# Optimization experiments

Hardware: AMD Instinct MI355X
Metric: run time of the kernel (lower is better)

The kernel has to match this reference:

```python
import jax, jax.numpy as jnp
import numpy as np

D = 512; N_HEAD = 8; D_HEAD = 64; D_INNER = 2048; SEG = 512; N_LAYER = 2; BATCH = 32
NUM_ITEMS = 50000
OMEGA = [2, 3, 4, 5, 7, 11, 21, 50]  # len == N_HEAD, required by multi-scale mask broadcast
EPS = 1e-8
STD = 0.02


def _layer_norm(x, w, b):
    mu = x.mean(-1, keepdims=True)
    var = ((x - mu) ** 2).mean(-1, keepdims=True)
    return (x - mu) / jnp.sqrt(var + EPS) * w + b


def _masks():
    # dir_mask: triu(ones, 1) (reverse=False); ms_mask[i,j,m] per omega band
    dir_mask = jnp.triu(jnp.ones((SEG, SEG), jnp.float32), 1)
    ms = np.stack([np.tri(SEG, SEG, o - 1) != np.tri(SEG, SEG, -o) for o in OMEGA], axis=-1)
    return dir_mask, jnp.asarray(ms)


def _pos_emb():
    freq = jnp.arange(0, D, 2, dtype=jnp.float32)
    inv_freq = 1.0 / jnp.power(10000.0, freq / D)
    pos_seq = jnp.arange(SEG, -SEG, -1.0, dtype=jnp.float32)  # length 2*SEG
    sinusoid = pos_seq[:, None] * inv_freq[None, :]
    return jnp.concatenate([jnp.sin(sinusoid), jnp.cos(sinusoid)], axis=-1)  # (2S, D)


def _rel_shift_bnij(x, klen):
    b, n, i, j2 = x.shape
    x = x.reshape(b, n, j2, i)[:, :, 1:, :].reshape(b, n, i, j2 - 1)
    return x[:, :, :, :klen]


def setup_inputs() -> dict:
    key = jax.random.key(0)
    ks = jax.random.split(key, 16)
    L = N_LAYER
    item_emb = STD * jax.random.normal(ks[0], (NUM_ITEMS + 1, D), jnp.float32)
    item_emb = item_emb.at[0].set(0.0)  # padding_idx=0
    proj = lambda k: STD * jax.random.normal(k, (L, D, N_HEAD, D_HEAD), jnp.float32)
    return {
        "input_ids": jax.random.randint(ks[1], (BATCH, SEG), 0, NUM_ITEMS + 1),
        "input_mask": jnp.zeros((BATCH, SEG), jnp.float32),
        "item_emb": item_emb,
        "Wq": proj(ks[2]), "Wk": proj(ks[3]), "Wv": proj(ks[4]),
        "Wr": proj(ks[5]), "Wo": proj(ks[6]),
        "r_r_bias": STD * jax.random.normal(ks[7], (L, N_HEAD, D_HEAD), jnp.float32),
        "r_w_bias": STD * jax.random.normal(ks[8], (L, N_HEAD, D_HEAD), jnp.float32),
        "ln_attn_w": jnp.ones((L, D), jnp.float32), "ln_attn_b": jnp.zeros((L, D), jnp.float32),
        "W1": STD * jax.random.normal(ks[9], (L, D, D_INNER), jnp.float32),
        "b1": jnp.zeros((L, D_INNER), jnp.float32),
        "W2": STD * jax.random.normal(ks[10], (L, D_INNER, D), jnp.float32),
        "b2": jnp.zeros((L, D), jnp.float32),
        "ln_ff_w": jnp.ones((L, D), jnp.float32), "ln_ff_b": jnp.zeros((L, D), jnp.float32),
    }


def reference(input_ids, input_mask, item_emb, Wq, Wk, Wv, Wr, Wo, r_r_bias, r_w_bias,
              ln_attn_w, ln_attn_b, W1, b1, W2, b2, ln_ff_w, ln_ff_b):
    ids = input_ids.T                      # (S, B)
    im = input_mask.T.astype(jnp.float32)  # (S, B)
    dir_mask, ms_mask = _masks()
    # data_mask: (q,k,b); attn_mask: (q,k,b,n) via multi-scale bands (training path)
    data_mask = im[None, :, :] + im[:, None, :] + dir_mask[:, :, None]
    attn_mask = ((data_mask[:, :, :, None] + (~ms_mask)[:, :, None, :].astype(jnp.float32)) > 0).astype(jnp.float32)
    mask_bnij = jnp.transpose(attn_mask, (2, 3, 0, 1))  # (b,n,i,j)

    h = item_emb[ids]          # (S, B, D)
    pos = _pos_emb()           # (2S, D), shared across batch
    scale = 1.0 / np.sqrt(D_HEAD).astype(np.float32)

    for l in range(N_LAYER):
        k_h = jnp.einsum('ibh,hnd->ibnd', h, Wk[l])
        v_h = jnp.einsum('ibh,hnd->ibnd', h, Wv[l])
        k_r = jnp.einsum('jh,hnd->jnd', pos, Wr[l])   # pos shared across batch
        q_h = jnp.einsum('ibh,hnd->ibnd', h, Wq[l])
        ac = jnp.einsum('ibnd,jbnd->bnij', q_h + r_w_bias[l], k_h)
        bd = jnp.einsum('ibnd,jnd->bnij', q_h + r_r_bias[l], k_r)
        bd = _rel_shift_bnij(bd, SEG)
        attn_score = (ac + bd) * scale - 1e30 * mask_bnij
        attn_prob = jax.nn.softmax(attn_score, axis=3)
        attn_vec = jnp.einsum('bnij,jbnd->ibnd', attn_prob, v_h)
        attn_out = jnp.einsum('ibnd,hnd->ibh', attn_vec, Wo[l])
        h = _layer_norm(attn_out + h, ln_attn_w[l], ln_attn_b[l])
        ff = jax.nn.gelu(h @ W1[l] + b1[l], approximate=False) @ W2[l] + b2[l]
        h = _layer_norm(ff + h, ln_ff_w[l], ln_ff_b[l])

    return jnp.transpose(h, (1, 0, 2))  # (B, S, D)
```

## Files before the change

kernel.cpp:

```cpp
#include <hip/hip_runtime.h>
#include <math.h>


#define S_  512
#define B_  32
#define D_  512
#define NH  8
#define DH  64
#define DI  2048
#define M_  (S_*B_)
#define QKV_LD 1536
#define WL  3407872
#define FP32_ONE 0x3F800000u

typedef unsigned short ushort_t;
typedef __attribute__((ext_vector_type(8))) short short8;
typedef __attribute__((ext_vector_type(4))) float f32x4;

__constant__ int OMEGA_C[8] = {2, 3, 4, 5, 7, 11, 21, 50};

__device__ __forceinline__ float b2f(ushort_t us) {
    return __uint_as_float(((unsigned int)us) << 16);
}
__device__ __forceinline__ ushort_t f2b(float f) {
    unsigned int u = __float_as_uint(f);
    return (ushort_t)((u + 0x7fffu + ((u >> 16) & 1u)) >> 16);
}
__device__ __forceinline__ float ldx(const void* p, size_t idx, bool isbf) {
    return isbf ? b2f(((const ushort_t*)p)[idx]) : ((const float*)p)[idx];
}
__device__ __forceinline__ void async16(const ushort_t* g, ushort_t* l) {
    __builtin_amdgcn_global_load_lds(
        (const __attribute__((address_space(1))) unsigned int*)g,
        (__attribute__((address_space(3))) unsigned int*)l, 16, 0, 0);
}

__device__ __forceinline__ float fast_gelu(float v) {
    float x  = v * 0.7071067811865475f;
    float ax = fabsf(x);
    float t  = __builtin_amdgcn_rcpf(fmaf(0.3275911f, ax, 1.f));
    float p  = fmaf(fmaf(fmaf(fmaf(1.061405429f, t, -1.453152027f),
                              t, 1.421413741f),
                         t, -0.284496736f),
                    t, 0.254829592f) * t;
    float e    = __expf(-ax * ax);
    float erfa = fmaf(-p, e, 1.f);
    float erfx = copysignf(erfa, x);
    return 0.5f * v * (1.f + erfx);
}

#define DPPA(v, ctrl) v += __int_as_float(__builtin_amdgcn_update_dpp(0, __float_as_int(v), ctrl, 0xf, 0xf, true))
__device__ __forceinline__ void dpp_sum64(float& v) {
    DPPA(v, 0x111); DPPA(v, 0x112); DPPA(v, 0x114);
    DPPA(v, 0x118); DPPA(v, 0x142); DPPA(v, 0x143);
}
#define DPPROR(v, ctrl) __int_as_float(__builtin_amdgcn_update_dpp(__float_as_int(v), __float_as_int(v), ctrl, 0xf, 0xf, false))
__device__ __forceinline__ float row16_sum(float v) {
    v += DPPROR(v, 0x128); v += DPPROR(v, 0x124);
    v += DPPROR(v, 0x122); v += DPPROR(v, 0x121);
    return v;
}
__device__ __forceinline__ float row16_max(float v) {
    v = fmaxf(v, DPPROR(v, 0x128)); v = fmaxf(v, DPPROR(v, 0x124));
    v = fmaxf(v, DPPROR(v, 0x122)); v = fmaxf(v, DPPROR(v, 0x121));
    return v;
}
__device__ __forceinline__ float rlane(float v, int l) {
    return __int_as_float(__builtin_amdgcn_readlane(__float_as_int(v), l));
}

__global__ __launch_bounds__(256) void embed_kernel(const int* __restrict__ ids,
                                                    const void* __restrict__ emb,
                                                    ushort_t* __restrict__ h,
                                                    const unsigned int* __restrict__ dtp) {
    const bool isbf = (dtp[0] != FP32_ONE);
    int idx = blockIdx.x * 256 + threadIdx.x;
    int d8 = idx & 63;
    int row = idx >> 6;
    int s = row >> 5, b = row & 31;
    int id = ids[b * S_ + s];
    size_t src = (size_t)id * D_ + d8 * 8;
    if (isbf) {
        *(uint4*)(h + (size_t)row * D_ + d8 * 8) = *(const uint4*)((const ushort_t*)emb + src);
    } else {
        const float* e = (const float*)emb + src;
        float4 a0 = ((const float4*)e)[0], a1 = ((const float4*)e)[1];
        uint4 pk;
        pk.x = (unsigned)f2b(a0.x) | ((unsigned)f2b(a0.y) << 16);
        pk.y = (unsigned)f2b(a0.z) | ((unsigned)f2b(a0.w) << 16);
        pk.z = (unsigned)f2b(a1.x) | ((unsigned)f2b(a1.y) << 16);
        pk.w = (unsigned)f2b(a1.z) | ((unsigned)f2b(a1.w) << 16);
        *(uint4*)(h + (size_t)row * D_ + d8 * 8) = pk;
    }
}

__global__ __launch_bounds__(256) void posemb_kernel(ushort_t* __restrict__ pos) {
    int flat = blockIdx.x * 256 + threadIdx.x;
    int p = flat >> 8, k = flat & 255;
    float inv = expf((float)k * -0.035977892078031f);
    float val = (512.0f - (float)p) * inv;
    pos[p * D_ + k]       = f2b(sinf(val));
    pos[p * D_ + 256 + k] = f2b(cosf(val));
}

__global__ __launch_bounds__(256) void transp_cvt4(
    const void* __restrict__ s0, const void* __restrict__ s1,
    const void* __restrict__ s2, const void* __restrict__ s3,
    ushort_t* __restrict__ wbuf, const unsigned int* __restrict__ dtp) {
    const bool isbf = (dtp[0] != FP32_ONE);
    __shared__ float tt[32][33];
    int z = blockIdx.z, layer = z >> 2, t4 = z & 3;
    const void* srcs[4] = {s0, s1, s2, s3};
    const void* in = srcs[t4];
    size_t inoff = (size_t)layer * 262144;
    ushort_t* out = wbuf + (size_t)layer * WL + (size_t)t4 * 262144;
    int tx = threadIdx.x & 31, ty = threadIdx.x >> 5;
    int n0 = blockIdx.x * 32, k0 = blockIdx.y * 32;
#pragma unroll
    for (int it = 0; it < 4; ++it)
        tt[ty + it * 8][tx] = ldx(in, inoff + (size_t)(k0 + ty + it * 8) * 512 + n0 + tx, isbf);
    __syncthreads();
#pragma unroll
    for (int it = 0; it < 4; ++it)
        out[(size_t)(n0 + ty + it * 8) * 512 + k0 + tx] = f2b(tt[tx][ty + it * 8]);
}

__global__ __launch_bounds__(256) void transp_cvtL(const void* __restrict__ in, size_t perlin,
                                                   ushort_t* __restrict__ wbuf, size_t outoff,
                                                   const unsigned int* __restrict__ dtp,
                                                   int K, int N) {
    const bool isbf = (dtp[0] != FP32_ONE);
    __shared__ float tt[32][33];
    int layer = blockIdx.z;
    size_t inoff = (size_t)layer * perlin;
    ushort_t* out = wbuf + (size_t)layer * WL + outoff;
    int tx = threadIdx.x & 31, ty = threadIdx.x >> 5;
    int n0 = blockIdx.x * 32, k0 = blockIdx.y * 32;
#pragma unroll
    for (int it = 0; it < 4; ++it)
        tt[ty + it * 8][tx] = ldx(in, inoff + (size_t)(k0 + ty + it * 8) * N + n0 + tx, isbf);
    __syncthreads();
#pragma unroll
    for (int it = 0; it < 4; ++it)
        out[(size_t)(n0 + ty + it * 8) * K + k0 + tx] = f2b(tt[tx][ty + it * 8]);
}

__global__ __launch_bounds__(256) void cvtL(const void* __restrict__ in, size_t perlin,
                                            ushort_t* __restrict__ wbuf, size_t outoff,
                                            const unsigned int* __restrict__ dtp, int nelem) {
    const bool isbf = (dtp[0] != FP32_ONE);
    int layer = blockIdx.z;
    int i = blockIdx.x * 256 + threadIdx.x;
    if (i < nelem)
        wbuf[(size_t)layer * WL + outoff + i] = f2b(ldx(in, (size_t)layer * perlin + i, isbf));
}

template<int EPI>
__global__ __launch_bounds__(256)
void mfma_gemm(const ushort_t* __restrict__ A, int lda,
               const ushort_t* __restrict__ Bt, int ldb,
               const void* __restrict__ biasv, size_t biasoff,
               ushort_t* __restrict__ C, int ldc,
               const unsigned int* __restrict__ dtp, int M, int N, int K) {
    const bool isbf = (dtp[0] != FP32_ONE);
    __shared__ ushort_t As[3][128 * 32];
    __shared__ ushort_t Bs[3][128 * 32];
    const int tid = threadIdx.x;
    const int nwg = gridDim.x * gridDim.y;
    const int wg  = blockIdx.y * gridDim.x + blockIdx.x;
    const int cpx = nwg >> 3;
    const int swz = (wg & 7) * cpx + (wg >> 3);
    const int bm = (swz / gridDim.y) * 128;
    const int bn = (swz % gridDim.y) * 128;
    const int w = tid >> 6, lane = tid & 63;
    const int wr = w >> 1, wc = w & 1;
    const int quad = lane >> 4, l16 = lane & 15;
    const int rsub = lane >> 2;
    const int kcg  = (lane & 3) ^ ((rsub >> 1) & 3);
    const int fsw  = (l16 >> 1) & 3;

    const ushort_t* ga0 = A  + (size_t)(bm + w * 16 + rsub) * lda + kcg * 8;
    const ushort_t* ga1 = A  + (size_t)(bm + (4 + w) * 16 + rsub) * lda + kcg * 8;
    const ushort_t* gb0 = Bt + (size_t)(bn + w * 16 + rsub) * ldb + kcg * 8;
    const ushort_t* gb1 = Bt + (size_t)(bn + (4 + w) * 16 + rsub) * ldb + kcg * 8;

#define STAGE_T(kt, bi) do {                                  \
        int _k0 = (kt) << 5;                                  \
        async16(ga0 + _k0, As[bi] + w * 512);                 \
        async16(gb0 + _k0, Bs[bi] + w * 512);                 \
        async16(ga1 + _k0, As[bi] + (4 + w) * 512);           \
        async16(gb1 + _k0, Bs[bi] + (4 + w) * 512);           \
    } while (0)

    f32x4 acc[4][4];
#pragma unroll
    for (int i = 0; i < 4; ++i)
#pragma unroll
        for (int j = 0; j < 4; ++j)
#pragma unroll
            for (int r = 0; r < 4; ++r) acc[i][j][r] = 0.f;

    const int nt = K >> 5;
    STAGE_T(0, 0);
    STAGE_T(1, 1);
    int cur = 0, nxt = 2;
    for (int t = 0; t < nt; ++t) {
        if (t + 2 < nt) {
            STAGE_T(t + 2, nxt);
            asm volatile("s_waitcnt vmcnt(8)" ::: "memory");
        } else if (t + 1 < nt) {
            asm volatile("s_waitcnt vmcnt(4)" ::: "memory");
        } else {
            asm volatile("s_waitcnt vmcnt(0)" ::: "memory");
        }
        __builtin_amdgcn_s_barrier();
        asm volatile("" ::: "memory");

        short8 af[4], bf[4];
#pragma unroll
        for (int tt = 0; tt < 4; ++tt) {
            int ra = wr * 64 + tt * 16 + l16;
            int rb = wc * 64 + tt * 16 + l16;
            af[tt] = *(const short8*)(As[cur] + ra * 32 + ((quad ^ fsw) * 8));
            bf[tt] = *(const short8*)(Bs[cur] + rb * 32 + ((quad ^ fsw) * 8));
        }
#pragma unroll
        for (int tr = 0; tr < 4; ++tr)
#pragma unroll
            for (int tc = 0; tc < 4; ++tc)
                acc[tr][tc] = __builtin_amdgcn_mfma_f32_16x16x32_bf16(bf[tc], af[tr], acc[tr][tc], 0, 0, 0);

        asm volatile("s_waitcnt lgkmcnt(0)" ::: "memory");
        __builtin_amdgcn_s_barrier();
        cur = cur == 2 ? 0 : cur + 1;
        nxt = nxt == 2 ? 0 : nxt + 1;
    }
#undef STAGE_T

    float bv[4][4];
    if (EPI >= 1) {
#pragma unroll
        for (int tc = 0; tc < 4; ++tc)
#pragma unroll
            for (int r = 0; r < 4; ++r)
                bv[tc][r] = ldx(biasv, biasoff + bn + wc * 64 + tc * 16 + quad * 4 + r, isbf);
    }
#pragma unroll
    for (int tr = 0; tr < 4; ++tr) {
        int grow = bm + wr * 64 + tr * 16 + l16;
#pragma unroll
        for (int tc = 0; tc < 4; ++tc) {
            int gcb = bn + wc * 64 + tc * 16 + quad * 4;
            float x[4];
#pragma unroll
            for (int r = 0; r < 4; ++r) {
                float v = acc[tr][tc][r];
                if (EPI >= 1) v += bv[tc][r];
                if (EPI == 2) v = fast_gelu(v);
                x[r] = v;
            }
            uint2 pk;
            pk.x = (unsigned)f2b(x[0]) | ((unsigned)f2b(x[1]) << 16);
            pk.y = (unsigned)f2b(x[2]) | ((unsigned)f2b(x[3]) << 16);
            *(uint2*)(C + (size_t)grow * ldc + gcb) = pk;
        }
    }
}

__global__ __launch_bounds__(256) void attn_mfma(
    ushort_t* __restrict__ qkv, const ushort_t* __restrict__ krb,
    const void* __restrict__ rwb, const void* __restrict__ rrb, size_t boff,
    const void* __restrict__ im,
    const unsigned int* __restrict__ dtp) {
    const bool isbf = (dtp[0] != FP32_ONE);
    __shared__ ushort_t Ks[128 * 64];
    __shared__ ushort_t VT[64 * 128];
    __shared__ ushort_t Rs[64 * 64];
    __shared__ float    BD2[4 * 16 * 64];
    __shared__ ushort_t Ps[4 * 16 * 128];
    __shared__ float    imk[128];
    __shared__ float    imq[64];

    const int tid = threadIdx.x;
    const int i0 = blockIdx.x * 64;
    const int b  = blockIdx.y;
    const int n  = blockIdx.z;
    const int o  = OMEGA_C[n];
    const int noff = n * DH;
    const int j0 = i0 - 64;
    const int w = tid >> 6, lane = tid & 63;
    const int quad = lane >> 4, l16 = lane & 15;

#pragma unroll
    for (int it = 0; it < 4; ++it) {
        int q4 = it * 256 + tid;
        int c  = q4 >> 3, ch = q4 & 7;
        int jc = j0 + c; jc = jc < 0 ? 0 : jc;
        size_t rowb = (size_t)(jc * B_ + b) * QKV_LD + noff;
        *(uint4*)(Ks + c * 64 + ((ch ^ (c & 7)) << 3)) = *(const uint4*)(qkv + rowb + 512 + ch * 8);
        ushort_t v8[8];
        *(uint4*)v8 = *(const uint4*)(qkv + rowb + 1024 + ch * 8);
#pragma unroll
        for (int e = 0; e < 8; ++e) {
            int vr = ch * 8 + e;
            VT[vr * 128 + (((c >> 3) ^ (vr & 15)) << 3) + (c & 7)] = v8[e];
        }
    }
#pragma unroll
    for (int it = 0; it < 2; ++it) {
        int q4 = it * 256 + tid;
        int m = q4 >> 3, ch = q4 & 7;
        *(uint4*)(Rs + m * 64 + ((ch ^ (m & 7)) << 3)) =
            *(const uint4*)(krb + (size_t)(512 - m) * 512 + noff + ch * 8);
    }
    if (tid < 128) {
        int j = j0 + tid;
        imk[tid] = (j >= 0) ? ldx(im, b * S_ + j, isbf) : 0.f;
    } else if (tid < 192) {
        imq[tid - 128] = ldx(im, b * S_ + i0 + (tid - 128), isbf);
    }
    __syncthreads();

    const int qrow = i0 + w * 16 + l16;
    size_t qbase = (size_t)(qrow * B_ + b) * QKV_LD + noff;
    short8 aw[2], ar[2];
#pragma unroll
    for (int kc = 0; kc < 2; ++kc) {
        int kof = kc * 32 + quad * 8;
        ushort_t qe[8];
        *(uint4*)qe = *(const uint4*)(qkv + qbase + kof);
#pragma unroll
        for (int e = 0; e < 8; ++e) {
            float f = b2f(qe[e]);
            ((ushort_t*)&aw[kc])[e] = f2b(f + ldx(rwb, boff + noff + kof + e, isbf));
            ((ushort_t*)&ar[kc])[e] = f2b(f + ldx(rrb, boff + noff + kof + e, isbf));
        }
    }

    f32x4 accs[8];
#pragma unroll
    for (int ct = 0; ct < 8; ++ct) {
        int kr = ct * 16 + l16;
        short8 b0 = *(const short8*)(Ks + kr * 64 + ((quad ^ (kr & 7)) << 3));
        short8 b1 = *(const short8*)(Ks + kr * 64 + (((quad + 4) ^ (kr & 7)) << 3));
        f32x4 z = {0.f, 0.f, 0.f, 0.f};
        z = __builtin_amdgcn_mfma_f32_16x16x32_bf16(aw[0], b0, z, 0, 0, 0);
        z = __builtin_amdgcn_mfma_f32_16x16x32_bf16(aw[1], b1, z, 0, 0, 0);
        accs[ct] = z;
    }
    float* BD2w = BD2 + w * 16 * 64;
#pragma unroll
    for (int mt = 0; mt < 4; ++mt) {
        int rr = mt * 16 + l16;
        short8 b0 = *(const short8*)(Rs + rr * 64 + ((quad ^ (rr & 7)) << 3));
        short8 b1 = *(const short8*)(Rs + rr * 64 + (((quad + 4) ^ (rr & 7)) << 3));
        f32x4 z = {0.f, 0.f, 0.f, 0.f};
        z = __builtin_amdgcn_mfma_f32_16x16x32_bf16(ar[0], b0, z, 0, 0, 0);
        z = __builtin_amdgcn_mfma_f32_16x16x32_bf16(ar[1], b1, z, 0, 0, 0);
#pragma unroll
        for (int r = 0; r < 4; ++r)
            BD2w[(quad * 4 + r) * 64 + mt * 16 + l16] = z[r];
    }

    float im_i[4];
#pragma unroll
    for (int r = 0; r < 4; ++r) im_i[r] = imq[w * 16 + quad * 4 + r];

    float sc[8][4];
#pragma unroll
    for (int ct = 0; ct < 8; ++ct) {
        int cl = ct * 16 + l16;
        float imk_c = imk[cl];
#pragma unroll
        for (int r = 0; r < 4; ++r) {
            int qrl = w * 16 + quad * 4 + r;
            int rel = qrl + 64 - cl;
            int relc = rel < 0 ? 0 : (rel > 63 ? 63 : rel);
            float bd = BD2w[(quad * 4 + r) * 64 + relc];
            bool valid = (rel >= 0) && (rel < o) && (rel <= i0 + qrl)
                         && (im_i[r] + imk_c <= 0.f);
            sc[ct][r] = valid ? (accs[ct][r] + bd) * 0.125f : -1e30f;
        }
    }
    float rl[4];
#pragma unroll
    for (int r = 0; r < 4; ++r) {
        float mx = sc[0][r];
#pragma unroll
        for (int ct = 1; ct < 8; ++ct) mx = fmaxf(mx, sc[ct][r]);
        mx = row16_max(mx);
        float l = 0.f;
#pragma unroll
        for (int ct = 0; ct < 8; ++ct) {
            float pv = __expf(sc[ct][r] - mx);
            sc[ct][r] = pv;
            l += pv;
        }
        l = row16_sum(l);
        rl[r] = 1.f / l;
    }
    ushort_t* Pw = Ps + w * 16 * 128;
#pragma unroll
    for (int ct = 0; ct < 8; ++ct)
#pragma unroll
        for (int r = 0; r < 4; ++r) {
            int prow = quad * 4 + r;
            Pw[prow * 128 + ((((ct * 2 + (l16 >> 3)) ^ prow) & 15) << 3) + (l16 & 7)]
                = f2b(sc[ct][r] * rl[r]);
        }

    short8 aP[4];
#pragma unroll
    for (int kc = 0; kc < 4; ++kc)
        aP[kc] = *(const short8*)(Pw + l16 * 128 + ((((kc * 4 + quad) ^ l16) & 15) << 3));

    const int qg = i0 + w * 16 + l16;
    const size_t obase = (size_t)(qg * B_ + b) * QKV_LD + noff;
#pragma unroll
    for (int dt = 0; dt < 4; ++dt) {
        f32x4 accT = {0.f, 0.f, 0.f, 0.f};
#pragma unroll
        for (int kc = 0; kc < 4; ++kc) {
            int vrow = dt * 16 + l16;
            short8 bV = *(const short8*)(VT + vrow * 128 + ((((kc * 4 + quad) ^ (vrow & 15)) & 15) << 3));
            accT = __builtin_amdgcn_mfma_f32_16x16x32_bf16(bV, aP[kc], accT, 0, 0, 0);
        }
        uint2 pk;
        pk.x = (unsigned)f2b(accT[0]) | ((unsigned)f2b(accT[1]) << 16);
        pk.y = (unsigned)f2b(accT[2]) | ((unsigned)f2b(accT[3]) << 16);
        *(uint2*)(qkv + obase + dt * 16 + quad * 4) = pk;
    }
}

__global__ __launch_bounds__(256) void add_ln_kernel(
    const ushort_t* __restrict__ x, ushort_t* __restrict__ h,
    const void* __restrict__ w, const void* __restrict__ b, size_t boff,
    const unsigned int* __restrict__ dtp) {
    const bool isbf = (dtp[0] != FP32_ONE);
    int lane = threadIdx.x & 63;
    int row = blockIdx.x * 4 + (threadIdx.x >> 6);
    size_t base = (size_t)row * D_ + lane * 8;
    ushort_t xe[8], he[8];
    *(uint4*)xe = *(const uint4*)(x + base);
    *(uint4*)he = *(const uint4*)(h + base);
    float v[8];
    float s = 0.f, ss = 0.f;
#pragma unroll
    for (int e = 0; e < 8; ++e) {
        v[e] = b2f(xe[e]) + b2f(he[e]);
        s += v[e]; ss += v[e] * v[e];
    }
    dpp_sum64(s); dpp_sum64(ss);
    float S = rlane(s, 63), SS = rlane(ss, 63);
    float mu  = S * (1.f / D_);
    float var = fmaxf(SS * (1.f / D_) - mu * mu, 0.f);
    float inv = rsqrtf(var + 1e-8f);
    ushort_t oe[8];
#pragma unroll
    for (int e = 0; e < 8; ++e)
        oe[e] = f2b((v[e] - mu) * inv * ldx(w, boff + lane * 8 + e, isbf)
                    + ldx(b, boff + lane * 8 + e, isbf));
    *(uint4*)(h + base) = *(uint4*)oe;
}

__global__ __launch_bounds__(256) void writeout_kernel(const ushort_t* __restrict__ h,
                                                       void* __restrict__ out,
                                                       const unsigned int* __restrict__ dtp) {
    const bool isbf = (dtp[0] != FP32_ONE);
    int idx = blockIdx.x * 256 + threadIdx.x;
    int d8 = idx & 63;
    int rest = idx >> 6;
    int s = rest & (S_ - 1), b = rest >> 9;
    ushort_t ve[8];
    *(uint4*)ve = *(const uint4*)(h + ((size_t)(s * B_ + b) << 9) + d8 * 8);
    if (isbf) {
        *(uint4*)((ushort_t*)out + (size_t)idx * 8) = *(uint4*)ve;
    } else {
        float* op = (float*)out + (size_t)idx * 8;
        ((float4*)op)[0] = make_float4(b2f(ve[0]), b2f(ve[1]), b2f(ve[2]), b2f(ve[3]));
        ((float4*)op)[1] = make_float4(b2f(ve[4]), b2f(ve[5]), b2f(ve[6]), b2f(ve[7]));
    }
}

extern "C" void kernel_launch(void* const* d_in, const int* in_sizes, int n_in,
                              void* d_out, int out_size, void* d_ws, size_t ws_size,
                              hipStream_t stream) {
    (void)in_sizes; (void)n_in; (void)out_size; (void)ws_size;
    const int*  ids = (const int*)d_in[0];
    const void* im  = d_in[1];
    const void* emb = d_in[2];
    const void* Wq = d_in[3], *Wk = d_in[4], *Wv = d_in[5], *Wr = d_in[6], *Wo = d_in[7];
    const void* rrb = d_in[8], *rwb = d_in[9];
    const void* lnaw = d_in[10], *lnab = d_in[11];
    const void* W1 = d_in[12], *b1 = d_in[13], *W2 = d_in[14], *b2 = d_in[15];
    const void* lnfw = d_in[16], *lnfb = d_in[17];
    const unsigned int* dtp = (const unsigned int*)d_in[10];

    char* wsb = (char*)d_ws;
    ushort_t* h    = (ushort_t*)wsb;
    ushort_t* qkv  = (ushort_t*)(wsb + (16u << 20));
    ushort_t* tmp  = (ushort_t*)(wsb + (64u << 20));
    ushort_t* ff1  = (ushort_t*)(wsb + (80u << 20));
    ushort_t* wbuf = (ushort_t*)(wsb + (144u << 20));
    ushort_t* posb = (ushort_t*)(wsb + (157u << 20));
    ushort_t* krb0 = (ushort_t*)(wsb + (158u << 20));
    ushort_t* krb1 = (ushort_t*)(wsb + (159u << 20));

    embed_kernel<<<4096, 256, 0, stream>>>(ids, emb, h, dtp);
    posemb_kernel<<<1024, 256, 0, stream>>>(posb);

    transp_cvt4<<<dim3(16, 16, 8), 256, 0, stream>>>(Wq, Wk, Wv, Wr, wbuf, dtp);
    cvtL<<<dim3(1024, 1, 2), 256, 0, stream>>>(Wo, 262144, wbuf, 1048576, dtp, 262144);
    transp_cvtL<<<dim3(64, 16, 2), 256, 0, stream>>>(W1, 1048576, wbuf, 1310720, dtp, 512, 2048);
    transp_cvtL<<<dim3(16, 64, 2), 256, 0, stream>>>(W2, 1048576, wbuf, 2359296, dtp, 2048, 512);

    mfma_gemm<0><<<dim3(8, 4), 256, 0, stream>>>(posb, 512, wbuf + 786432, 512, nullptr, 0, krb0, 512, dtp, 1024, 512, 512);
    mfma_gemm<0><<<dim3(8, 4), 256, 0, stream>>>(posb, 512, wbuf + WL + 786432, 512, nullptr, 0, krb1, 512, dtp, 1024, 512, 512);

    for (int l = 0; l < 2; ++l) {
        size_t boff = (size_t)l * 512;
        size_t b1off = (size_t)l * 2048;
        ushort_t* qkvT = wbuf + (size_t)l * WL;
        ushort_t* woc  = qkvT + 1048576;
        ushort_t* w1T  = woc  + 262144;
        ushort_t* w2T  = w1T  + 1048576;
        ushort_t* krb  = l ? krb1 : krb0;

        mfma_gemm<0><<<dim3(128, 12), 256, 0, stream>>>(h, 512, qkvT, 512, nullptr, 0, qkv, QKV_LD, dtp, M_, QKV_LD, 512);

        attn_mfma<<<dim3(8, 32, 8), 256, 0, stream>>>(qkv, krb, rwb, rrb, boff, im, dtp);

        mfma_gemm<0><<<dim3(128, 4), 256, 0, stream>>>(qkv, QKV_LD, woc, 512, nullptr, 0, tmp, 512, dtp, M_, 512, 512);
        add_ln_kernel<<<4096, 256, 0, stream>>>(tmp, h, lnaw, lnab, boff, dtp);

        mfma_gemm<2><<<dim3(128, 16), 256, 0, stream>>>(h, 512, w1T, 512, b1, b1off, ff1, DI, dtp, M_, DI, 512);
        mfma_gemm<1><<<dim3(128, 4),  256, 0, stream>>>(ff1, DI, w2T, 2048, b2, boff, tmp, 512, dtp, M_, 512, DI);
        add_ln_kernel<<<4096, 256, 0, stream>>>(tmp, h, lnfw, lnfb, boff, dtp);
    }

    writeout_kernel<<<4096, 256, 0, stream>>>(h, d_out, dtp);
}
```

Measured before the change: 762.5 us.

## Add 256x256-tile 8-wave GEMM with swizzled grid for QKV and FFN1

```diff
diff --git a/kernel.cpp b/kernel.cpp
--- a/kernel.cpp
+++ b/kernel.cpp
@@ -267,6 +267,154 @@
     }
 }
 
+template<int EPI>
+__global__ __launch_bounds__(512, 2)
+void mfma_gemm256(const ushort_t* __restrict__ A, int lda,
+                  const ushort_t* __restrict__ Bt, int ldb,
+                  const void* __restrict__ biasv, size_t biasoff,
+                  ushort_t* __restrict__ C, int ldc,
+                  const unsigned int* __restrict__ dtp, int N, int K) {
+    __shared__ ushort_t As[2][256 * 64];
+    __shared__ ushort_t Bs[2][256 * 64];
+    const int tid = threadIdx.x;
+    const int nwg = gridDim.x * gridDim.y;
+    const int wg  = blockIdx.y * gridDim.x + blockIdx.x;
+    const int cpx = nwg >> 3;
+    const int swz = (wg & 7) * cpx + (wg >> 3);
+    const int bm = (swz / gridDim.y) * 256;
+    const int bn = (swz % gridDim.y) * 256;
+    const int wid = tid >> 6, lane = tid & 63;
+    const int wr = wid >> 2, wc = wid & 3;
+    const int quad = lane >> 4, l16 = lane & 15;
+    const int l7 = l16 & 7;
+
+    const int srow = tid >> 3;
+    const int sch  = (tid & 7) ^ (srow & 7);
+    const int ldsoff0 = tid * 8, ldsoff1 = (512 + tid) * 8;
+
+#define STAGE256(X) do {                                                       \
+        int ts_ = (X) >> 2, j2_ = (X) & 3, b_ = ts_ & 1;                       \
+        if (j2_ < 2) {                                                         \
+            const ushort_t* g0 = A + (size_t)(bm + j2_ * 128 + srow) * lda     \
+                                 + ts_ * 64 + sch * 8;                         \
+            async16(g0,             As[b_] + j2_ * 8192 + ldsoff0);            \
+            async16(g0 + 64 * lda,  As[b_] + j2_ * 8192 + ldsoff1);            \
+        } else {                                                               \
+            const ushort_t* g0 = Bt + (size_t)(bn + (j2_ - 2) * 128 + srow) * ldb \
+                                 + ts_ * 64 + sch * 8;                         \
+            async16(g0,             Bs[b_] + (j2_ - 2) * 8192 + ldsoff0);      \
+            async16(g0 + 64 * ldb,  Bs[b_] + (j2_ - 2) * 8192 + ldsoff1);      \
+        }                                                                      \
+    } while (0)
+
+    f32x4 acc[8][4];
+#pragma unroll
+    for (int i = 0; i < 8; ++i)
+#pragma unroll
+        for (int j = 0; j < 4; ++j)
+#pragma unroll
+            for (int r = 0; r < 4; ++r) acc[i][j][r] = 0.f;
+
+    const int NT = K >> 6;
+    STAGE256(0); STAGE256(1); STAGE256(2); STAGE256(3); STAGE256(4);
+    asm volatile("s_waitcnt vmcnt(2)" ::: "memory");
+    __builtin_amdgcn_s_barrier();
+
+    const int arow = wr * 128 + l16;
+    const int brow = wc * 64 + l16;
+    const int chq0 = (quad ^ l7) * 8;
+    const int chq1 = ((4 + quad) ^ l7) * 8;
+
+    short8 af[4][2], bf[4][2];
+    for (int kt = 0; kt < NT; ++kt) {
+        const ushort_t* Ab = As[kt & 1];
+        const ushort_t* Bb = Bs[kt & 1];
+#pragma unroll
+        for (int j = 0; j < 4; ++j) {
+            const int rh = j >> 1, nh = j & 1;
+            if (j == 0) {
+#pragma unroll
+                for (int m = 0; m < 4; ++m) {
+                    const ushort_t* rp = Ab + (arow + m * 16) * 64;
+                    af[m][0] = *(const short8*)(rp + chq0);
+                    af[m][1] = *(const short8*)(rp + chq1);
+                }
+#pragma unroll
+                for (int n2 = 0; n2 < 2; ++n2) {
+                    const ushort_t* rp = Bb + (brow + n2 * 16) * 64;
+                    bf[n2][0] = *(const short8*)(rp + chq0);
+                    bf[n2][1] = *(const short8*)(rp + chq1);
+                }
+            } else if (j == 1) {
+#pragma unroll
+                for (int n2 = 0; n2 < 2; ++n2) {
+                    const ushort_t* rp = Bb + (brow + (2 + n2) * 16) * 64;
+                    bf[2 + n2][0] = *(const short8*)(rp + chq0);
+                    bf[2 + n2][1] = *(const short8*)(rp + chq1);
+                }
+            } else if (j == 2) {
+#pragma unroll
+                for (int m = 0; m < 4; ++m) {
+                    const ushort_t* rp = Ab + (arow + 64 + m * 16) * 64;
+                    af[m][0] = *(const short8*)(rp + chq0);
+                    af[m][1] = *(const short8*)(rp + chq1);
+                }
+            }
+            int hg = kt * 4 + j + 5;
+            if (hg < NT * 4) STAGE256(hg);
+            __builtin_amdgcn_s_barrier();
+            __builtin_amdgcn_s_setprio(1);
+#pragma unroll
+            for (int m = 0; m < 4; ++m)
+#pragma unroll
+                for (int n2 = 0; n2 < 2; ++n2) {
+                    f32x4 a = acc[rh * 4 + m][nh * 2 + n2];
+                    a = __builtin_amdgcn_mfma_f32_16x16x32_bf16(bf[nh * 2 + n2][0], af[m][0], a, 0, 0, 0);
+                    a = __builtin_amdgcn_mfma_f32_16x16x32_bf16(bf[nh * 2 + n2][1], af[m][1], a, 0, 0, 0);
+                    acc[rh * 4 + m][nh * 2 + n2] = a;
+                }
+            __builtin_amdgcn_s_setprio(0);
+            if (j == 3 && kt + 1 < NT) {
+                if (kt + 3 < NT) asm volatile("s_waitcnt vmcnt(2)" ::: "memory");
+                else             asm volatile("s_waitcnt vmcnt(0)" ::: "memory");
+            }
+            __builtin_amdgcn_s_barrier();
+        }
+    }
+#undef STAGE256
+
+    const bool isbf = (dtp[0] != FP32_ONE);
+    float bv[4][4];
+    if (EPI >= 1) {
+#pragma unroll
+        for (int ni = 0; ni < 4; ++ni)
+#pragma unroll
+            for (int r = 0; r < 4; ++r)
+                bv[ni][r] = ldx(biasv, biasoff + bn + wc * 64 + ni * 16 + quad * 4 + r, isbf);
+    }
+    (void)N;
+#pragma unroll
+    for (int mi = 0; mi < 8; ++mi) {
+        int grow = bm + wr * 128 + mi * 16 + l16;
+#pragma unroll
+        for (int ni = 0; ni < 4; ++ni) {
+            int gcb = bn + wc * 64 + ni * 16 + quad * 4;
+            float x[4];
+#pragma unroll
+            for (int r = 0; r < 4; ++r) {
+                float v = acc[mi][ni][r];
+                if (EPI >= 1) v += bv[ni][r];
+                if (EPI == 2) v = fast_gelu(v);
+                x[r] = v;
+            }
+            uint2 pk;
+            pk.x = (unsigned)f2b(x[0]) | ((unsigned)f2b(x[1]) << 16);
+            pk.y = (unsigned)f2b(x[2]) | ((unsigned)f2b(x[3]) << 16);
+            *(uint2*)(C + (size_t)grow * ldc + gcb) = pk;
+        }
+    }
+}
+
 __global__ __launch_bounds__(256) void attn_mfma(
     ushort_t* __restrict__ qkv, const ushort_t* __restrict__ krb,
     const void* __restrict__ rwb, const void* __restrict__ rrb, size_t boff,
@@ -526,14 +674,14 @@
         ushort_t* w2T  = w1T  + 1048576;
         ushort_t* krb  = l ? krb1 : krb0;
 
-        mfma_gemm<0><<<dim3(128, 12), 256, 0, stream>>>(h, 512, qkvT, 512, nullptr, 0, qkv, QKV_LD, dtp, M_, QKV_LD, 512);
+        mfma_gemm256<0><<<dim3(64, 6), 512, 0, stream>>>(h, 512, qkvT, 512, nullptr, 0, qkv, QKV_LD, dtp, QKV_LD, 512);
 
         attn_mfma<<<dim3(8, 32, 8), 256, 0, stream>>>(qkv, krb, rwb, rrb, boff, im, dtp);
 
         mfma_gemm<0><<<dim3(128, 4), 256, 0, stream>>>(qkv, QKV_LD, woc, 512, nullptr, 0, tmp, 512, dtp, M_, 512, 512);
         add_ln_kernel<<<4096, 256, 0, stream>>>(tmp, h, lnaw, lnab, boff, dtp);
 
-        mfma_gemm<2><<<dim3(128, 16), 256, 0, stream>>>(h, 512, w1T, 512, b1, b1off, ff1, DI, dtp, M_, DI, 512);
+        mfma_gemm256<2><<<dim3(64, 8), 512, 0, stream>>>(h, 512, w1T, 512, b1, b1off, ff1, DI, dtp, DI, 512);
         mfma_gemm<1><<<dim3(128, 4),  256, 0, stream>>>(ff1, DI, w2T, 2048, b2, boff, tmp, 512, dtp, M_, 512, DI);
         add_ln_kernel<<<4096, 256, 0, stream>>>(tmp, h, lnfw, lnfb, boff, dtp);
     }
```

Result: no change. 772.0 us (+1.2%).
